# Performance work log

Measured on AMD Instinct MI355X. Metric: run time of the kernel, lower is better.

Reference implementation:

```python
import jax, jax.numpy as jnp
import numpy as np

N1, N2, N3 = 40000, 30000, 30000
N = N1 + N2 + N3          # total nodes after vstack
E = 800000                # edges
D_IN = 256                # in_channels
D_HID = 256               # 2 * out_channels
D_OUT = 128               # out_channels


def _glorot(k, shape):
    lim = (6.0 / (shape[0] + shape[1])) ** 0.5
    return jax.random.uniform(k, shape, jnp.float32, -lim, lim)


def setup_inputs() -> dict:
    key = jax.random.key(0)
    ks = jax.random.split(key, 12)
    x1 = jax.random.normal(ks[0], (N1, 128), jnp.float32)
    x2 = jax.random.normal(ks[1], (N2, 256), jnp.float32)
    x3 = jax.random.normal(ks[2], (N3, 64), jnp.float32)
    edge_index = jax.random.randint(ks[3], (2, E), 0, N, jnp.int64)
    return {
        "x1": x1, "x2": x2, "x3": x3,
        "Wp1": _glorot(ks[4], (128, D_IN)), "bp1": jnp.zeros((D_IN,), jnp.float32),
        "Wp2": _glorot(ks[5], (256, D_IN)), "bp2": jnp.zeros((D_IN,), jnp.float32),
        "Wp3": _glorot(ks[6], (64, D_IN)),  "bp3": jnp.zeros((D_IN,), jnp.float32),
        "W1": _glorot(ks[7], (D_IN, D_HID)), "b1": jnp.zeros((D_HID,), jnp.float32),
        "W2": _glorot(ks[8], (D_HID, D_OUT)), "b2": jnp.zeros((D_OUT,), jnp.float32),
        "edge_index": edge_index,
    }


def _gcn_conv(x, W, b, src, dst, dis):
    # PyG GCNConv: h = xW; out[j] = sum_i norm_ij * h[i] (incl. self-loop) + b
    h = x @ W                                   # [N, d_out]
    msg = h[src] * (dis[src] * dis[dst])[:, None]   # [E, d_out] edge messages
    agg = jax.ops.segment_sum(msg, dst, num_segments=N)
    agg = agg + h * (dis * dis)[:, None]        # self-loop term (norm = 1/deg)
    return agg + b


def reference(x1, x2, x3, Wp1, bp1, Wp2, bp2, Wp3, bp3, W1, b1, W2, b2, edge_index):
    # per-type projection + vstack
    x = jnp.concatenate([x1 @ Wp1 + bp1, x2 @ Wp2 + bp2, x3 @ Wp3 + bp3], axis=0)
    # dropout(p=0.5) is identity in eval mode (deterministic baseline)
    src, dst = edge_index[0], edge_index[1]
    # degree with self-loops (in-degree at dst, as in PyG gcn_norm)
    deg = jnp.ones((N,), x.dtype).at[dst].add(1.0)
    dis = jax.lax.rsqrt(deg)                    # deg^{-1/2}
    h = jax.nn.relu(_gcn_conv(x, W1, b1, src, dst, dis))
    return _gcn_conv(h, W2, b2, src, dst, dis)
```

## Files before the change

kernel.cpp:

```cpp
#include <hip/hip_runtime.h>
#include <cstddef>

#define NT 100000
#define NN1 40000
#define NN2 30000
#define NN3 30000
#define EE 800000

typedef _Float16 f16;
typedef f16 f16x8 __attribute__((ext_vector_type(8)));
typedef f16 f16x4 __attribute__((ext_vector_type(4)));
typedef float f32x4 __attribute__((ext_vector_type(4)));

static inline int cdiv(int a, int b) { return (a + b - 1) / b; }

__device__ __forceinline__ void gload_lds16(const f16* g, f16* l) {
    __builtin_amdgcn_global_load_lds(
        (const __attribute__((address_space(1))) void*)g,
        (__attribute__((address_space(3))) void*)l, 16, 0, 0);
}

__global__ void k_scan1(const int* __restrict__ cnt, int* __restrict__ rowptr,
                        int* __restrict__ part, float* __restrict__ dis, int n) {
    __shared__ int sums[256];
    int b = blockIdx.x, t = threadIdx.x;
    int base = b * 1024 + t * 4;
    int v0 = (base + 0 < n) ? cnt[base + 0] : 0;
    int v1 = (base + 1 < n) ? cnt[base + 1] : 0;
    int v2 = (base + 2 < n) ? cnt[base + 2] : 0;
    int v3 = (base + 3 < n) ? cnt[base + 3] : 0;
    if (base + 0 < n) dis[base + 0] = rsqrtf((float)v0 + 1.0f);
    if (base + 1 < n) dis[base + 1] = rsqrtf((float)v1 + 1.0f);
    if (base + 2 < n) dis[base + 2] = rsqrtf((float)v2 + 1.0f);
    if (base + 3 < n) dis[base + 3] = rsqrtf((float)v3 + 1.0f);
    int tsum = v0 + v1 + v2 + v3;
    sums[t] = tsum;
    __syncthreads();
    for (int off = 1; off < 256; off <<= 1) {
        int y = (t >= off) ? sums[t - off] : 0;
        __syncthreads();
        sums[t] += y;
        __syncthreads();
    }
    int excl = sums[t] - tsum;
    if (base + 0 < n) rowptr[base + 0] = excl;
    if (base + 1 < n) rowptr[base + 1] = excl + v0;
    if (base + 2 < n) rowptr[base + 2] = excl + v0 + v1;
    if (base + 3 < n) rowptr[base + 3] = excl + v0 + v1 + v2;
    if (t == 255) part[b] = sums[255];
}

__global__ void k_scan2(int* __restrict__ part, int nb) {
    __shared__ int sums[256];
    int t = threadIdx.x;
    int v = (t < nb) ? part[t] : 0;
    sums[t] = v;
    __syncthreads();
    for (int off = 1; off < 256; off <<= 1) {
        int y = (t >= off) ? sums[t - off] : 0;
        __syncthreads();
        sums[t] += y;
        __syncthreads();
    }
    if (t < nb) part[t] = sums[t] - v;
}

__global__ void k_scan3(int* __restrict__ rowptr, const int* __restrict__ part,
                        int n, int total) {
    int i = blockIdx.x * blockDim.x + threadIdx.x;
    if (i < n) rowptr[i] += part[i >> 10];
    if (i == 0) rowptr[n] = total;
}

struct TArgs {
    const float *W0, *W1, *W2, *W3, *W4;
    f16 *T0, *T1, *T2, *T3, *T4;
};
#define HB   3125
#define CVTB 14375
#define TRB  832
#define NA4  1280000
#define NB4  1920000
#define NC4  480000
struct PrepArgs {
    const int* dst; int* cnt;
    const float *x1, *x2, *x3; f16* xc;
    TArgs t;
};
__global__ __launch_bounds__(256) void k_prep(PrepArgs a) {
    int bid = blockIdx.x, tid = threadIdx.x;
    if (bid < HB) {
        int i = bid * 256 + tid;
        if (i < EE) atomicAdd(&a.cnt[a.dst[i]], 1);
    } else if (bid < HB + CVTB) {
        int i = (bid - HB) * 256 + tid;
        const float* s; int j;
        if (i < NA4) { s = a.x1; j = i; }
        else if (i < NA4 + NB4) { s = a.x2; j = i - NA4; }
        else if (i < NA4 + NB4 + NC4) { s = a.x3; j = i - NA4 - NB4; }
        else return;
        float4 v = reinterpret_cast<const float4*>(s)[j];
        f16x4 r = {(f16)v.x, (f16)v.y, (f16)v.z, (f16)v.w};
        reinterpret_cast<f16x4*>(a.xc)[i] = r;
    } else {
        int i = (bid - HB - CVTB) * 256 + tid;
        const float* W; f16* T; int K, N, j;
        if      (i <  32768) { W = a.t.W0; T = a.t.T0; K = 128; N = 256; j = i; }
        else if (i <  98304) { W = a.t.W1; T = a.t.T1; K = 256; N = 256; j = i - 32768; }
        else if (i < 114688) { W = a.t.W2; T = a.t.T2; K =  64; N = 256; j = i - 98304; }
        else if (i < 180224) { W = a.t.W3; T = a.t.T3; K = 256; N = 256; j = i - 114688; }
        else if (i < 212992) { W = a.t.W4; T = a.t.T4; K = 256; N = 128; j = i - 180224; }
        else return;
        int k = j / N, n = j - k * N;
        T[n * K + k] = (f16)W[j];
    }
}

template<bool RELU_OUT, bool HAS_BIAS>
__device__ __forceinline__
void hgemm_body(f16* As, f16* Bs,
                const f16* __restrict__ A, const f16* __restrict__ BT,
                const float* __restrict__ bias, f16* __restrict__ C,
                int M, int K, int N, int bx, int by) {
    const int tid = threadIdx.x;
    const int lane = tid & 63;
    const int wid = tid >> 6;
    const int wm = wid & 1, wn = wid >> 1;
    const int bm = bx * 128;
    const int bn = by * 128;
    const int r15 = lane & 15, g = lane >> 4;
    const int sr  = lane >> 2;
    const int chs = (lane & 3) ^ ((lane >> 3) & 3);

    auto stage = [&](int buf, int k0) {
        #pragma unroll
        for (int q = 0; q < 2; ++q) {
            int chunk = wid + q * 4;
            int row = chunk * 16 + sr;
            int ga = bm + row; if (ga >= M) ga = M - 1;
            gload_lds16(A  + (size_t)ga * K + k0 + chs * 8, As + buf * 4096 + chunk * 512);
            gload_lds16(BT + (size_t)(bn + row) * K + k0 + chs * 8, Bs + buf * 4096 + chunk * 512);
        }
    };

    f32x4 acc[4][4] = {};
    const int nsteps = K >> 5;
    stage(0, 0);
    __syncthreads();
    int cur = 0;
    for (int step = 0; step < nsteps; ++step) {
        if (step + 1 < nsteps) stage(cur ^ 1, (step + 1) << 5);
        f16x8 af[4], bf[4];
        const int sl = (g ^ ((r15 >> 1) & 3)) * 8;
        #pragma unroll
        for (int mf = 0; mf < 4; ++mf) {
            int row = wm * 64 + mf * 16 + r15;
            af[mf] = *reinterpret_cast<const f16x8*>(As + cur * 4096 + row * 32 + sl);
        }
        #pragma unroll
        for (int nf = 0; nf < 4; ++nf) {
            int row = wn * 64 + nf * 16 + r15;
            bf[nf] = *reinterpret_cast<const f16x8*>(Bs + cur * 4096 + row * 32 + sl);
        }
        #pragma unroll
        for (int mf = 0; mf < 4; ++mf)
            #pragma unroll
            for (int nf = 0; nf < 4; ++nf)
                acc[mf][nf] = __builtin_amdgcn_mfma_f32_16x16x32_f16(af[mf], bf[nf], acc[mf][nf], 0, 0, 0);
        __syncthreads();
        cur ^= 1;
    }

    #pragma unroll
    for (int mf = 0; mf < 4; ++mf) {
        #pragma unroll
        for (int nf = 0; nf < 4; ++nf) {
            int col = bn + wn * 64 + nf * 16 + r15;
            float bv = HAS_BIAS ? bias[col] : 0.f;
            #pragma unroll
            for (int r = 0; r < 4; ++r) {
                int rowg = bm + wm * 64 + mf * 16 + g * 4 + r;
                if (rowg < M) {
                    float v = acc[mf][nf][r] + bv;
                    if (RELU_OUT) v = fmaxf(v, 0.f);
                    C[(size_t)rowg * N + col] = (f16)v;
                }
            }
        }
    }
}

struct P3 {
    const f16 *a1, *a2, *a3, *t1, *t2, *t3;
    const float *b1, *b2, *b3;
    f16 *o1, *o2, *o3;
    int g1, g2;
};
#define FB 3125
struct FPArgs {
    const int *src, *dst;
    const float* dis;
    const int* rowptr;
    int* cursor;
    int2* e_pairs;
    P3 p;
};
__global__ __launch_bounds__(256) void k_fillproj(FPArgs a) {
    extern __shared__ f16 smem[];
    int bid = blockIdx.x;
    if (bid < FB) {
        int i = bid * 256 + threadIdx.x;
        if (i >= EE) return;
        int s = a.src[i], t = a.dst[i];
        int pos = atomicAdd(&a.cursor[t], 1);
        int2 pr;
        pr.x = s;
        pr.y = __float_as_int(a.dis[s] * a.dis[t]);
        a.e_pairs[a.rowptr[t] + pos] = pr;
    } else {
        int pb = bid - FB;
        int bx = pb >> 1, by = pb & 1;
        if (bx < a.p.g1)
            hgemm_body<false, true>(smem, smem + 8192, a.p.a1, a.p.t1, a.p.b1, a.p.o1, NN1, 128, 256, bx, by);
        else if (bx < a.p.g1 + a.p.g2)
            hgemm_body<false, true>(smem, smem + 8192, a.p.a2, a.p.t2, a.p.b2, a.p.o2, NN2, 256, 256, bx - a.p.g1, by);
        else
            hgemm_body<false, true>(smem, smem + 8192, a.p.a3, a.p.t3, a.p.b3, a.p.o3, NN3, 64, 256, bx - a.p.g1 - a.p.g2, by);
    }
}

__global__ __launch_bounds__(512)
void k_fused(const f16* __restrict__ x16, const float* __restrict__ dis,
             const int* __restrict__ rowptr, const int2* __restrict__ e_pairs,
             const f16* __restrict__ W1T, const float* __restrict__ b1,
             const f16* __restrict__ W2T, f16* __restrict__ hw2, int M) {
    __shared__ f16 P[64 * 256];
    const int tid = threadIdx.x;
    const int lane = tid & 63;
    const int bm = blockIdx.x * 64;

    {
        const int grp = tid >> 5;
        const int l = tid & 31;
        #pragma unroll
        for (int it = 0; it < 4; ++it) {
            int row = it * 16 + grp;
            int node = bm + row;
            float av[8];
            if (node < M) {
                float dj = dis[node];
                int r0 = rowptr[node], r1 = rowptr[node + 1];
                int deg = r1 - r0;
                int si = 0; float wi = 0.f;
                if (l < deg) { int2 pr = e_pairs[r0 + l]; si = pr.x; wi = __int_as_float(pr.y); }
                f16x8 sa = reinterpret_cast<const f16x8*>(x16 + (size_t)node * 256)[l];
                float wself = dj * dj;
                #pragma unroll
                for (int k = 0; k < 8; ++k) av[k] = (float)sa[k] * wself;
                int n32 = deg < 32 ? deg : 32;
                int e = 0;
                for (; e + 8 <= n32; e += 8) {
                    int s[8]; float w[8];
                    #pragma unroll
                    for (int q = 0; q < 8; ++q) {
                        s[q] = __shfl(si, e + q, 32);
                        w[q] = __shfl(wi, e + q, 32);
                    }
                    f16x8 u[8];
                    #pragma unroll
                    for (int q = 0; q < 8; ++q)
                        u[q] = reinterpret_cast<const f16x8*>(x16 + (size_t)s[q] * 256)[l];
                    #pragma unroll
                    for (int q = 0; q < 8; ++q)
                        #pragma unroll
                        for (int k = 0; k < 8; ++k) av[k] += (float)u[q][k] * w[q];
                }
                for (; e + 4 <= n32; e += 4) {
                    int s[4]; float w[4];
                    #pragma unroll
                    for (int q = 0; q < 4; ++q) {
                        s[q] = __shfl(si, e + q, 32);
                        w[q] = __shfl(wi, e + q, 32);
                    }
                    f16x8 u[4];
                    #pragma unroll
                    for (int q = 0; q < 4; ++q)
                        u[q] = reinterpret_cast<const f16x8*>(x16 + (size_t)s[q] * 256)[l];
                    #pragma unroll
                    for (int q = 0; q < 4; ++q)
                        #pragma unroll
                        for (int k = 0; k < 8; ++k) av[k] += (float)u[q][k] * w[q];
                }
                for (; e < n32; ++e) {
                    int s0 = __shfl(si, e, 32);
                    float w0 = __shfl(wi, e, 32);
                    f16x8 u0 = reinterpret_cast<const f16x8*>(x16 + (size_t)s0 * 256)[l];
                    #pragma unroll
                    for (int k = 0; k < 8; ++k) av[k] += (float)u0[k] * w0;
                }
                for (int e2 = r0 + 32; e2 < r1; ++e2) {
                    int2 pr = e_pairs[e2];
                    float w0 = __int_as_float(pr.y);
                    f16x8 u0 = reinterpret_cast<const f16x8*>(x16 + (size_t)pr.x * 256)[l];
                    #pragma unroll
                    for (int k = 0; k < 8; ++k) av[k] += (float)u0[k] * w0;
                }
            } else {
                #pragma unroll
                for (int k = 0; k < 8; ++k) av[k] = 0.f;
            }
            f16x8 r;
            #pragma unroll
            for (int k = 0; k < 8; ++k) r[k] = (f16)av[k];
            int slot = (l & 3) ^ ((row >> 1) & 3);
            *reinterpret_cast<f16x8*>(P + (l >> 2) * 2048 + row * 32 + slot * 8) = r;
        }
    }
    __syncthreads();

    const int w = tid >> 6;
    const int r15 = lane & 15, g = lane >> 4;
    f32x4 acc[4][2] = {};
    for (int step = 0; step < 8; ++step) {
        f16x8 af[4], bf[2];
        #pragma unroll
        for (int mf = 0; mf < 4; ++mf) {
            int row = mf * 16 + r15;
            int slot = g ^ ((row >> 1) & 3);
            af[mf] = *reinterpret_cast<const f16x8*>(P + step * 2048 + row * 32 + slot * 8);
        }
        #pragma unroll
        for (int nf = 0; nf < 2; ++nf) {
            int n1 = w * 32 + nf * 16 + r15;
            bf[nf] = *reinterpret_cast<const f16x8*>(W1T + (size_t)n1 * 256 + step * 32 + g * 8);
        }
        #pragma unroll
        for (int mf = 0; mf < 4; ++mf)
            #pragma unroll
            for (int nf = 0; nf < 2; ++nf)
                acc[mf][nf] = __builtin_amdgcn_mfma_f32_16x16x32_f16(af[mf], bf[nf], acc[mf][nf], 0, 0, 0);
    }
    __syncthreads();

    #pragma unroll
    for (int nf = 0; nf < 2; ++nf) {
        int col = w * 32 + nf * 16 + r15;
        float bv = b1[col];
        int gp = (col >> 3) & 3, c7 = col & 7;
        #pragma unroll
        for (int mf = 0; mf < 4; ++mf) {
            #pragma unroll
            for (int rr = 0; rr < 4; ++rr) {
                int row = mf * 16 + g * 4 + rr;
                float v = fmaxf(acc[mf][nf][rr] + bv, 0.f);
                int slot = gp ^ ((row >> 1) & 3);
                P[w * 2048 + row * 32 + slot * 8 + c7] = (f16)v;
            }
        }
    }
    __syncthreads();

    f32x4 acc2[4] = {};
    for (int step = 0; step < 8; ++step) {
        f16x8 af[4], bf;
        #pragma unroll
        for (int mf = 0; mf < 4; ++mf) {
            int row = mf * 16 + r15;
            int slot = g ^ ((row >> 1) & 3);
            af[mf] = *reinterpret_cast<const f16x8*>(P + step * 2048 + row * 32 + slot * 8);
        }
        int n2 = w * 16 + r15;
        bf = *reinterpret_cast<const f16x8*>(W2T + (size_t)n2 * 256 + step * 32 + g * 8);
        #pragma unroll
        for (int mf = 0; mf < 4; ++mf)
            acc2[mf] = __builtin_amdgcn_mfma_f32_16x16x32_f16(af[mf], bf, acc2[mf], 0, 0, 0);
    }

    #pragma unroll
    for (int mf = 0; mf < 4; ++mf) {
        int col = w * 16 + r15;
        #pragma unroll
        for (int rr = 0; rr < 4; ++rr) {
            int rowg = bm + mf * 16 + g * 4 + rr;
            if (rowg < M)
                hw2[(size_t)rowg * 128 + col] = (f16)acc2[mf][rr];
        }
    }
}

__global__ void k_gather128(const f16* __restrict__ f, const float* __restrict__ dis,
                            const int* __restrict__ rowptr, const int2* __restrict__ e_pairs,
                            const float* __restrict__ bias, float* __restrict__ outb, int n) {
    int node = (int)(((long long)blockIdx.x * blockDim.x + threadIdx.x) >> 5);
    int l = threadIdx.x & 31;
    if (node >= n) return;
    float dj = dis[node];
    int r0 = rowptr[node], r1 = rowptr[node + 1];
    int deg = r1 - r0;
    int si = 0; float wi = 0.f;
    if (l < deg) { int2 p = e_pairs[r0 + l]; si = p.x; wi = __int_as_float(p.y); }
    f16x4 a = reinterpret_cast<const f16x4*>(f + (size_t)node * 128)[l];
    float wsf = dj * dj;
    float acc[4];
    #pragma unroll
    for (int k = 0; k < 4; ++k) acc[k] = (float)a[k] * wsf;
    int n32 = deg < 32 ? deg : 32;
    int e = 0;
    for (; e + 8 <= n32; e += 8) {
        int s[8]; float w[8];
        #pragma unroll
        for (int q = 0; q < 8; ++q) {
            s[q] = __shfl(si, e + q, 32);
            w[q] = __shfl(wi, e + q, 32);
        }
        f16x4 u[8];
        #pragma unroll
        for (int q = 0; q < 8; ++q)
            u[q] = reinterpret_cast<const f16x4*>(f + (size_t)s[q] * 128)[l];
        #pragma unroll
        for (int q = 0; q < 8; ++q)
            #pragma unroll
            for (int k = 0; k < 4; ++k) acc[k] += (float)u[q][k] * w[q];
    }
    for (; e + 4 <= n32; e += 4) {
        int s[4]; float w[4];
        #pragma unroll
        for (int q = 0; q < 4; ++q) {
            s[q] = __shfl(si, e + q, 32);
            w[q] = __shfl(wi, e + q, 32);
        }
        f16x4 u[4];
        #pragma unroll
        for (int q = 0; q < 4; ++q)
            u[q] = reinterpret_cast<const f16x4*>(f + (size_t)s[q] * 128)[l];
        #pragma unroll
        for (int q = 0; q < 4; ++q)
            #pragma unroll
            for (int k = 0; k < 4; ++k) acc[k] += (float)u[q][k] * w[q];
    }
    for (; e < n32; ++e) {
        int s0 = __shfl(si, e, 32);
        float w0 = __shfl(wi, e, 32);
        f16x4 u0 = reinterpret_cast<const f16x4*>(f + (size_t)s0 * 128)[l];
        #pragma unroll
        for (int k = 0; k < 4; ++k) acc[k] += (float)u0[k] * w0;
    }
    for (int e2 = r0 + 32; e2 < r1; ++e2) {
        int2 p = e_pairs[e2];
        float w0 = __int_as_float(p.y);
        f16x4 u0 = reinterpret_cast<const f16x4*>(f + (size_t)p.x * 128)[l];
        #pragma unroll
        for (int k = 0; k < 4; ++k) acc[k] += (float)u0[k] * w0;
    }
    float4 bb = reinterpret_cast<const float4*>(bias)[l];
    float4 r = make_float4(acc[0] + bb.x, acc[1] + bb.y, acc[2] + bb.z, acc[3] + bb.w);
    reinterpret_cast<float4*>(outb + (size_t)node * 128)[l] = r;
}

extern "C" void kernel_launch(void* const* d_in, const int* in_sizes, int n_in,
                              void* d_out, int out_size, void* d_ws, size_t ws_size,
                              hipStream_t stream) {
    const float* x1  = (const float*)d_in[0];
    const float* x2  = (const float*)d_in[1];
    const float* x3  = (const float*)d_in[2];
    const float* Wp1 = (const float*)d_in[3];
    const float* bp1 = (const float*)d_in[4];
    const float* Wp2 = (const float*)d_in[5];
    const float* bp2 = (const float*)d_in[6];
    const float* Wp3 = (const float*)d_in[7];
    const float* bp3 = (const float*)d_in[8];
    const float* W1  = (const float*)d_in[9];
    const float* b1  = (const float*)d_in[10];
    const float* W2  = (const float*)d_in[11];
    const float* b2  = (const float*)d_in[12];
    const int*   ei  = (const int*)d_in[13];
    const int* src = ei;
    const int* dst = ei + EE;
    float* out = (float*)d_out;

    char* ws = (char*)d_ws;
    size_t off = 0;
    auto alloc = [&](size_t bytes) {
        char* p = ws + off;
        off += (bytes + 511) & ~(size_t)511;
        return p;
    };
    float* dis    = (float*)alloc((size_t)NT * 4);
    int*   cnt    = (int*)alloc((size_t)NT * 4);
    int*   cursor = (int*)alloc((size_t)NT * 4);
    int*   rowptr = (int*)alloc((size_t)(NT + 1) * 4);
    int*   part   = (int*)alloc(256 * 4);
    int2*  e_pairs= (int2*)alloc((size_t)EE * 8);
    f16*   x16    = (f16*)alloc((size_t)NT * 256 * 2);
    f16*   hw216  = (f16*)alloc((size_t)NT * 128 * 2);
    f16*   xc     = (f16*)alloc((size_t)(NN1 * 128 + NN2 * 256 + NN3 * 64) * 2);
    f16*   Wp1T   = (f16*)alloc((size_t)256 * 128 * 2);
    f16*   Wp2T   = (f16*)alloc((size_t)256 * 256 * 2);
    f16*   Wp3T   = (f16*)alloc((size_t)256 * 64 * 2);
    f16*   W1T    = (f16*)alloc((size_t)256 * 256 * 2);
    f16*   W2T    = (f16*)alloc((size_t)128 * 256 * 2);

    f16* x1c = xc;
    f16* x2c = xc + (size_t)NN1 * 128;
    f16* x3c = xc + (size_t)NN1 * 128 + (size_t)NN2 * 256;

    const int nb = cdiv(NT, 1024);

    size_t zspan = (size_t)((char*)rowptr - (char*)cnt);
    hipMemsetAsync(cnt, 0, zspan, stream);

    {
        PrepArgs a;
        a.dst = dst; a.cnt = cnt;
        a.x1 = x1; a.x2 = x2; a.x3 = x3; a.xc = xc;
        a.t = {Wp1, Wp2, Wp3, W1, W2, Wp1T, Wp2T, Wp3T, W1T, W2T};
        k_prep<<<HB + CVTB + TRB, 256, 0, stream>>>(a);
    }

    k_scan1<<<nb, 256, 0, stream>>>(cnt, rowptr, part, dis, NT);
    k_scan2<<<1, 256, 0, stream>>>(part, nb);
    k_scan3<<<cdiv(NT, 256), 256, 0, stream>>>(rowptr, part, NT, EE);

    {
        FPArgs a;
        a.src = src; a.dst = dst; a.dis = dis; a.rowptr = rowptr;
        a.cursor = cursor; a.e_pairs = e_pairs;
        a.p = {x1c, x2c, x3c, Wp1T, Wp2T, Wp3T, bp1, bp2, bp3,
               x16, x16 + (size_t)NN1 * 256, x16 + (size_t)(NN1 + NN2) * 256,
               cdiv(NN1, 128), cdiv(NN2, 128)};
        int projb = (cdiv(NN1, 128) + cdiv(NN2, 128) + cdiv(NN3, 128)) * 2;
        k_fillproj<<<FB + projb, 256, 32768, stream>>>(a);
    }

    k_fused<<<cdiv(NT, 64), 512, 0, stream>>>(x16, dis, rowptr, e_pairs,
                                              W1T, b1, W2T, hw216, NT);

    k_gather128<<<cdiv(NT * 32, 256), 256, 0, stream>>>(hw216, dis, rowptr, e_pairs, b2, out, NT);
}
```

Measured before the change: 277.3 us.

## Gather neighbor rows with full wavefronts pulled from a dynamic LDS work queue

The aggregation phase of the fused kernel now assigns each node row to a full 64-lane wavefront, with each lane loading 4 halves instead of 8, rather than a 32-lane half-wave. Rows are claimed dynamically through an LDS atomic counter instead of a fixed 4-iterations-per-group schedule. The intent is to balance the uneven per-node degree across wavefronts and to cover up to 64 edges in the shuffle-broadcast fast path. The costs are narrower 8-byte loads per lane, one atomic per row, and the removal of the 4-edge unrolled tail loop.

```diff
diff --git a/kernel.cpp b/kernel.cpp
--- a/kernel.cpp
+++ b/kernel.cpp
@@ -235,86 +235,72 @@
              const f16* __restrict__ W1T, const float* __restrict__ b1,
              const f16* __restrict__ W2T, f16* __restrict__ hw2, int M) {
     __shared__ f16 P[64 * 256];
+    __shared__ int qhead;
     const int tid = threadIdx.x;
     const int lane = tid & 63;
     const int bm = blockIdx.x * 64;
 
-    {
-        const int grp = tid >> 5;
-        const int l = tid & 31;
-        #pragma unroll
-        for (int it = 0; it < 4; ++it) {
-            int row = it * 16 + grp;
-            int node = bm + row;
-            float av[8];
-            if (node < M) {
-                float dj = dis[node];
-                int r0 = rowptr[node], r1 = rowptr[node + 1];
-                int deg = r1 - r0;
-                int si = 0; float wi = 0.f;
-                if (l < deg) { int2 pr = e_pairs[r0 + l]; si = pr.x; wi = __int_as_float(pr.y); }
-                f16x8 sa = reinterpret_cast<const f16x8*>(x16 + (size_t)node * 256)[l];
-                float wself = dj * dj;
+    if (tid == 0) qhead = 0;
+    __syncthreads();
+
+    while (true) {
+        int row;
+        if (lane == 0) row = atomicAdd(&qhead, 1);
+        row = __shfl(row, 0);
+        if (row >= 64) break;
+        int node = bm + row;
+        float av[4];
+        if (node < M) {
+            float dj = dis[node];
+            int r0 = rowptr[node], r1 = rowptr[node + 1];
+            int deg = r1 - r0;
+            int si = 0; float wi = 0.f;
+            if (lane < deg) { int2 pr = e_pairs[r0 + lane]; si = pr.x; wi = __int_as_float(pr.y); }
+            f16x4 sa = reinterpret_cast<const f16x4*>(x16 + (size_t)node * 256)[lane];
+            float wself = dj * dj;
+            #pragma unroll
+            for (int k = 0; k < 4; ++k) av[k] = (float)sa[k] * wself;
+            int n64 = deg < 64 ? deg : 64;
+            int e = 0;
+            for (; e + 8 <= n64; e += 8) {
+                int s[8]; float w[8];
                 #pragma unroll
-                for (int k = 0; k < 8; ++k) av[k] = (float)sa[k] * wself;
-                int n32 = deg < 32 ? deg : 32;
-                int e = 0;
-                for (; e + 8 <= n32; e += 8) {
-                    int s[8]; float w[8];
+                for (int q = 0; q < 8; ++q) {
+                    s[q] = __shfl(si, e + q);
+                    w[q] = __shfl(wi, e + q);
+                }
+                f16x4 u[8];
+                #pragma unroll
+                for (int q = 0; q < 8; ++q)
+                    u[q] = reinterpret_cast<const f16x4*>(x16 + (size_t)s[q] * 256)[lane];
+                #pragma unroll
+                for (int q = 0; q < 8; ++q)
                     #pragma unroll
-                    for (int q = 0; q < 8; ++q) {
-                        s[q] = __shfl(si, e + q, 32);
-                        w[q] = __shfl(wi, e + q, 32);
-                    }
-                    f16x8 u[8];
-                    #pragma unroll
-                    for (int q = 0; q < 8; ++q)
-                        u[q] = reinterpret_cast<const f16x8*>(x16 + (size_t)s[q] * 256)[l];
-                    #pragma unroll
-                    for (int q = 0; q < 8; ++q)
-                        #pragma unroll
-                        for (int k = 0; k < 8; ++k) av[k] += (float)u[q][k] * w[q];
-                }
-                for (; e + 4 <= n32; e += 4) {
-                    int s[4]; float w[4];
-                    #pragma unroll
-                    for (int q = 0; q < 4; ++q) {
-                        s[q] = __shfl(si, e + q, 32);
-                        w[q] = __shfl(wi, e + q, 32);
-                    }
-                    f16x8 u[4];
-                    #pragma unroll
-                    for (int q = 0; q < 4; ++q)
-                        u[q] = reinterpret_cast<const f16x8*>(x16 + (size_t)s[q] * 256)[l];
-                    #pragma unroll
-                    for (int q = 0; q < 4; ++q)
-                        #pragma unroll
-                        for (int k = 0; k < 8; ++k) av[k] += (float)u[q][k] * w[q];
-                }
-                for (; e < n32; ++e) {
-                    int s0 = __shfl(si, e, 32);
-                    float w0 = __shfl(wi, e, 32);
-                    f16x8 u0 = reinterpret_cast<const f16x8*>(x16 + (size_t)s0 * 256)[l];
-                    #pragma unroll
-                    for (int k = 0; k < 8; ++k) av[k] += (float)u0[k] * w0;
-                }
-                for (int e2 = r0 + 32; e2 < r1; ++e2) {
-                    int2 pr = e_pairs[e2];
-                    float w0 = __int_as_float(pr.y);
-                    f16x8 u0 = reinterpret_cast<const f16x8*>(x16 + (size_t)pr.x * 256)[l];
-                    #pragma unroll
-                    for (int k = 0; k < 8; ++k) av[k] += (float)u0[k] * w0;
-                }
-            } else {
+                    for (int k = 0; k < 4; ++k) av[k] += (float)u[q][k] * w[q];
+            }
+            for (; e < n64; ++e) {
+                int s0 = __shfl(si, e);
+                float w0 = __shfl(wi, e);
+                f16x4 u0 = reinterpret_cast<const f16x4*>(x16 + (size_t)s0 * 256)[lane];
                 #pragma unroll
-                for (int k = 0; k < 8; ++k) av[k] = 0.f;
+                for (int k = 0; k < 4; ++k) av[k] += (float)u0[k] * w0;
             }
-            f16x8 r;
-            #pragma unroll
-            for (int k = 0; k < 8; ++k) r[k] = (f16)av[k];
-            int slot = (l & 3) ^ ((row >> 1) & 3);
-            *reinterpret_cast<f16x8*>(P + (l >> 2) * 2048 + row * 32 + slot * 8) = r;
-        }
+            for (int e2 = r0 + 64; e2 < r1; ++e2) {
+                int2 pr = e_pairs[e2];
+                float w0 = __int_as_float(pr.y);
+                f16x4 u0 = reinterpret_cast<const f16x4*>(x16 + (size_t)pr.x * 256)[lane];
+                #pragma unroll
+                for (int k = 0; k < 4; ++k) av[k] += (float)u0[k] * w0;
+            }
+        } else {
+            #pragma unroll
+            for (int k = 0; k < 4; ++k) av[k] = 0.f;
+        }
+        f16x4 r;
+        #pragma unroll
+        for (int k = 0; k < 4; ++k) r[k] = (f16)av[k];
+        int slot = ((lane >> 1) & 3) ^ ((row >> 1) & 3);
+        *reinterpret_cast<f16x4*>(P + (lane >> 3) * 2048 + row * 32 + slot * 8 + 4 * (lane & 1)) = r;
     }
     __syncthreads();
 
```

After: 298.9 us. 7.8% more time.
